# Kernel optimization log

Measured on AMD Instinct MI355X. Metric: run time of the kernel, lower is better.

Reference implementation:

```python
import jax, jax.numpy as jnp
import numpy as np

N = 100000      # nodes
E = 1600000     # edges
F_IN = 64       # CFG.feature_dim
H = 128         # CFG.hidden_dim
G = 128         # graphs in batch
LN_EPS = 1e-5


def setup_inputs() -> dict:
    key = jax.random.key(0)
    ks = jax.random.split(key, 12)
    x = jax.random.normal(ks[0], (N, F_IN), dtype=jnp.float32)
    edge_index = jax.random.randint(ks[1], (2, E), 0, N)
    batch = jnp.sort(jax.random.randint(ks[2], (N,), 0, G))
    # GCNConv weights (glorot-ish scale) and biases
    W1 = jax.random.normal(ks[3], (F_IN, H), dtype=jnp.float32) * (1.0 / np.sqrt(F_IN))
    b1 = jnp.zeros((H,), jnp.float32)
    W2 = jax.random.normal(ks[4], (H, H), dtype=jnp.float32) * (1.0 / np.sqrt(H))
    b2 = jnp.zeros((H,), jnp.float32)
    # LayerNorm affine params
    g1 = jnp.ones((H,), jnp.float32)
    beta1 = jnp.zeros((H,), jnp.float32)
    g2 = jnp.ones((H,), jnp.float32)
    beta2 = jnp.zeros((H,), jnp.float32)
    return {"x": x, "edge_index": edge_index, "batch": batch,
            "W1": W1, "b1": b1, "g1": g1, "beta1": beta1,
            "W2": W2, "b2": b2, "g2": g2, "beta2": beta2,
            "num_graphs": G}


def _gcn_conv(h, W, b, src, dst, n):
    """PyG GCNConv: add self-loops, symmetric D^-1/2 (A+I) D^-1/2 (h W) + b."""
    hw = h @ W                                   # [n, out]
    loop = jnp.arange(n, dtype=src.dtype)
    s = jnp.concatenate([src, loop])             # [E+n]
    d = jnp.concatenate([dst, loop])
    deg = jax.ops.segment_sum(jnp.ones_like(s, jnp.float32), d, num_segments=n)
    dinv = jax.lax.rsqrt(jnp.maximum(deg, 1e-12))
    norm = dinv[s] * dinv[d]                     # [E+n]
    msg = hw[s] * norm[:, None]                  # gather + scale
    out = jax.ops.segment_sum(msg, d, num_segments=n)
    return out + b


def _layer_norm(h, gamma, beta):
    mu = jnp.mean(h, axis=-1, keepdims=True)
    var = jnp.mean(jnp.square(h - mu), axis=-1, keepdims=True)
    return (h - mu) * jax.lax.rsqrt(var + LN_EPS) * gamma + beta


def reference(x, edge_index, batch, W1, b1, g1, beta1, W2, b2, g2, beta2, num_graphs):
    src, dst = edge_index[0], edge_index[1]
    n = x.shape[0]
    h = _gcn_conv(x, W1, b1, src, dst, n)
    h = _layer_norm(h, g1, beta1)
    h = jax.nn.relu(h)
    h = _gcn_conv(h, W2, b2, src, dst, n)
    h = _layer_norm(h, g2, beta2)
    # is_inverted defaults to False -> no sign flip
    sums = jax.ops.segment_sum(h, batch, num_segments=num_graphs)      # [G, H]
    counts = jax.ops.segment_sum(jnp.ones((n,), jnp.float32), batch, num_segments=num_graphs)
    return sums / jnp.maximum(counts, 1.0)[:, None]
```

## Files before the change

### kernel.cpp

```cpp
#include <hip/hip_runtime.h>
#include <hip/hip_bf16.h>

#define LN_EPS 1e-5f

typedef __attribute__((ext_vector_type(8))) short short8v;
typedef __attribute__((ext_vector_type(4))) float float4v;

__device__ __forceinline__ float bflo(unsigned u) { return __uint_as_float(u << 16); }
__device__ __forceinline__ float bfhi(unsigned u) { return __uint_as_float(u & 0xffff0000u); }
__device__ __forceinline__ unsigned pack2(float x, float y) {
    __hip_bfloat162 t = __float22bfloat162_rn(make_float2(x, y));
    return *reinterpret_cast<unsigned*>(&t);
}
__device__ __forceinline__ void add8(float* a, uint4 u) {
    a[0] += bflo(u.x); a[1] += bfhi(u.x);
    a[2] += bflo(u.y); a[3] += bfhi(u.y);
    a[4] += bflo(u.z); a[5] += bfhi(u.z);
    a[6] += bflo(u.w); a[7] += bfhi(u.w);
}

union U4S8 { uint4 u; short8v s; };


#define CHUNK 4096
#define NBMAX 512
#define BCAP 5120

__launch_bounds__(256)
__global__ void k_bucket(const int* __restrict__ src, const int* __restrict__ dst, int e,
                         int* __restrict__ gcnt, unsigned* __restrict__ stage) {
    __shared__ unsigned ebuf[CHUNK];
    __shared__ unsigned short ebkt[CHUNK];
    __shared__ int hist[NBMAX];
    __shared__ int base[NBMAX];
    int tid = threadIdx.x;
    int c0 = blockIdx.x * CHUNK;
    if (c0 >= e) return;
    int cnt = min(CHUNK, e - c0);

    for (int t = tid; t < NBMAX; t += 256) hist[t] = 0;
    __syncthreads();
    for (int t = tid; t < cnt; t += 256) {
        unsigned s = (unsigned)src[c0 + t];
        unsigned d = (unsigned)dst[c0 + t];
        ebuf[t] = s | ((d & 0xffu) << 24);
        ebkt[t] = (unsigned short)(d >> 8);
        atomicAdd(&hist[d >> 8], 1);
    }
    __syncthreads();
    for (int b = tid; b < NBMAX; b += 256) {
        int h = hist[b];
        if (h > 0) base[b] = b * BCAP + atomicAdd(&gcnt[b], h);
    }
    __syncthreads();
    for (int t = tid; t < cnt; t += 256) {
        int p = atomicAdd(&base[ebkt[t]], 1);
        stage[p] = ebuf[t];
    }
}

__launch_bounds__(256)
__global__ void k_csr(const unsigned* __restrict__ stage, const int* __restrict__ gcnt,
                      int* __restrict__ csr_src, int* __restrict__ row_start,
                      int* __restrict__ row_end, float* __restrict__ dinv,
                      const float* __restrict__ x, unsigned* __restrict__ xb, int n) {
    __shared__ int cntl[256];
    __shared__ int sc[256];
    __shared__ int excl[256];
    __shared__ float dfl[256];
    int b = blockIdx.x;
    int lo = b << 8;
    int nn = min(n - lo, 256);
    int tid = threadIdx.x;
    int s0 = b * BCAP;
    int cntB = gcnt[b];

    cntl[tid] = 0;
    __syncthreads();
    for (int t = tid; t < cntB; t += 256) {
        int dl = (int)(stage[s0 + t] >> 24);
        atomicAdd(&cntl[dl], 1);
    }
    __syncthreads();
    int deg = (tid < nn) ? cntl[tid] : 0;
    sc[tid] = deg; __syncthreads();
    for (int o = 1; o < 256; o <<= 1) {
        int t = (tid >= o) ? sc[tid - o] : 0;
        __syncthreads();
        sc[tid] += t;
        __syncthreads();
    }
    excl[tid] = sc[tid] - deg;
    float dv = rsqrtf((float)(deg + 1));
    dfl[tid] = dv;
    if (tid < nn) {
        row_start[lo + tid] = s0 + excl[tid];
        row_end[lo + tid]   = s0 + excl[tid] + deg;
        dinv[lo + tid] = dv;
    }
    cntl[tid] = 0;
    __syncthreads();
    for (int t = tid; t < cntB; t += 256) {
        unsigned ed = stage[s0 + t];
        int dl = (int)(ed >> 24);
        int r = atomicAdd(&cntl[dl], 1);
        csr_src[s0 + excl[dl] + r] = (int)(ed & 0x00ffffffu);
    }

    const float4* x4 = (const float4*)x;
    uint2* xb2 = (uint2*)xb;
    for (int idx = tid; idx < nn * 16; idx += 256) {
        int node = idx >> 4, c = idx & 15;
        size_t p = ((size_t)(lo + node) << 4) + c;
        float4 v = x4[p];
        float d = dfl[node];
        xb2[p] = make_uint2(pack2(v.x * d, v.y * d), pack2(v.z * d, v.w * d));
    }
}

__global__ void k_rc(const int* __restrict__ batch, int n, float* __restrict__ rc) {
    int g = threadIdx.x;
    int lo = 0, hi = n;
    while (lo < hi) { int m = (lo + hi) >> 1; if (batch[m] < g) lo = m + 1; else hi = m; }
    int st = lo;
    hi = n;
    while (lo < hi) { int m = (lo + hi) >> 1; if (batch[m] < g + 1) lo = m + 1; else hi = m; }
    rc[g] = 1.f / fmaxf((float)(lo - st), 1.f);
}


__global__ void k_agg64b(const uint4* __restrict__ x4, const float* __restrict__ dinv,
                         const int* __restrict__ row_start, const int* __restrict__ row_end,
                         const int* __restrict__ csr_src, uint4* __restrict__ out4, int n) {
    int lane = threadIdx.x & 63;
    int g = lane >> 3, c = lane & 7;
    int wid = (blockIdx.x * blockDim.x + threadIdx.x) >> 6;
    int nw = (gridDim.x * blockDim.x) >> 6;
    for (int i = wid; i < n; i += nw) {
        float a[8] = {0.f, 0.f, 0.f, 0.f, 0.f, 0.f, 0.f, 0.f};
        if (g == 0) {
            uint4 su = x4[(size_t)i * 8 + c];
            add8(a, su);
        }
        int j0 = row_start[i], j1 = row_end[i];
        int j = j0 + g;
        for (; j + 8 < j1; j += 16) {
            int s0 = csr_src[j], s1 = csr_src[j + 8];
            uint4 u0 = x4[(size_t)s0 * 8 + c];
            uint4 u1 = x4[(size_t)s1 * 8 + c];
            add8(a, u0);
            add8(a, u1);
        }
        if (j < j1) {
            int s0 = csr_src[j];
            uint4 u0 = x4[(size_t)s0 * 8 + c];
            add8(a, u0);
        }
        #pragma unroll
        for (int k = 0; k < 8; ++k) {
            a[k] += __shfl_xor(a[k], 8);
            a[k] += __shfl_xor(a[k], 16);
            a[k] += __shfl_xor(a[k], 32);
        }
        if (g == 0) {
            float di = dinv[i];
            uint4 o;
            o.x = pack2(a[0] * di, a[1] * di);
            o.y = pack2(a[2] * di, a[3] * di);
            o.z = pack2(a[4] * di, a[5] * di);
            o.w = pack2(a[6] * di, a[7] * di);
            out4[(size_t)i * 8 + c] = o;
        }
    }
}

__global__ void k_agg128b(const uint4* __restrict__ h4, const float* __restrict__ dinv,
                          const int* __restrict__ row_start, const int* __restrict__ row_end,
                          const int* __restrict__ csr_src, uint4* __restrict__ out4, int n) {
    int lane = threadIdx.x & 63;
    int q = lane >> 4, c = lane & 15;
    int wid = (blockIdx.x * blockDim.x + threadIdx.x) >> 6;
    int nw = (gridDim.x * blockDim.x) >> 6;
    for (int i = wid; i < n; i += nw) {
        float a[8] = {0.f, 0.f, 0.f, 0.f, 0.f, 0.f, 0.f, 0.f};
        if (q == 0) {
            uint4 su = h4[(size_t)i * 16 + c];
            add8(a, su);
        }
        int j0 = row_start[i], j1 = row_end[i];
        int j = j0 + q;
        for (; j + 12 < j1; j += 16) {
            int s0 = csr_src[j], s1 = csr_src[j + 4];
            int s2 = csr_src[j + 8], s3 = csr_src[j + 12];
            uint4 u0 = h4[(size_t)s0 * 16 + c];
            uint4 u1 = h4[(size_t)s1 * 16 + c];
            uint4 u2 = h4[(size_t)s2 * 16 + c];
            uint4 u3 = h4[(size_t)s3 * 16 + c];
            add8(a, u0);
            add8(a, u1);
            add8(a, u2);
            add8(a, u3);
        }
        for (; j < j1; j += 4) {
            int s0 = csr_src[j];
            uint4 u0 = h4[(size_t)s0 * 16 + c];
            add8(a, u0);
        }
        #pragma unroll
        for (int k = 0; k < 8; ++k) {
            a[k] += __shfl_xor(a[k], 16);
            a[k] += __shfl_xor(a[k], 32);
        }
        if (q == 0) {
            float di = dinv[i];
            uint4 o;
            o.x = pack2(a[0] * di, a[1] * di);
            o.y = pack2(a[2] * di, a[3] * di);
            o.z = pack2(a[4] * di, a[5] * di);
            o.w = pack2(a[6] * di, a[7] * di);
            out4[(size_t)i * 16 + c] = o;
        }
    }
}


__launch_bounds__(256)
__global__ void k_mm1(const unsigned* __restrict__ aggb, const float* __restrict__ W1,
                      const float* __restrict__ b1, const float* __restrict__ g1,
                      const float* __restrict__ be1, const float* __restrict__ dinv,
                      uint4* __restrict__ hb4, int ntiles) {
    __shared__ uint4 sB[2 * 8 * 64];
    for (int idx = threadIdx.x; idx < 1024; idx += blockDim.x) {
        int l = idx & 63;
        int f = idx >> 6;
        int ks = f >> 3, cb = f & 7;
        int kb = ks * 32 + (l >> 4) * 8;
        int col = cb * 16 + (l & 15);
        float p[8];
        #pragma unroll
        for (int j = 0; j < 8; ++j) p[j] = W1[(kb + j) * 128 + col];
        uint4 v;
        v.x = pack2(p[0], p[1]); v.y = pack2(p[2], p[3]);
        v.z = pack2(p[4], p[5]); v.w = pack2(p[6], p[7]);
        sB[idx] = v;
    }
    __syncthreads();

    int lane = threadIdx.x & 63;
    int wv = threadIdx.x >> 6;
    int wpb = blockDim.x >> 6;
    int lc = lane & 15, lg = lane >> 4;

    U4S8 B[2][8];
    #pragma unroll
    for (int ks = 0; ks < 2; ++ks)
        #pragma unroll
        for (int cb = 0; cb < 8; ++cb)
            B[ks][cb].u = sB[(ks * 8 + cb) * 64 + lane];

    float bs[8], gm[8], bt[8];
    #pragma unroll
    for (int cb = 0; cb < 8; ++cb) {
        bs[cb] = b1[cb * 16 + lc];
        gm[cb] = g1[cb * 16 + lc];
        bt[cb] = be1[cb * 16 + lc];
    }

    for (int t = blockIdx.x * wpb + wv; t < ntiles; t += gridDim.x * wpb) {
        size_t arow = (size_t)(t * 16 + lc) * 32;
        U4S8 a0, a1;
        a0.u = *(const uint4*)&aggb[arow + lg * 4];
        a1.u = *(const uint4*)&aggb[arow + 16 + lg * 4];
        float4v acc[8];
        #pragma unroll
        for (int cb = 0; cb < 8; ++cb) acc[cb] = (float4v){0.f, 0.f, 0.f, 0.f};
        #pragma unroll
        for (int cb = 0; cb < 8; ++cb) {
            acc[cb] = __builtin_amdgcn_mfma_f32_16x16x32_bf16(a0.s, B[0][cb].s, acc[cb], 0, 0, 0);
            acc[cb] = __builtin_amdgcn_mfma_f32_16x16x32_bf16(a1.s, B[1][cb].s, acc[cb], 0, 0, 0);
        }
        #pragma unroll
        for (int reg = 0; reg < 4; ++reg) {
            float s = 0.f, q = 0.f;
            #pragma unroll
            for (int cb = 0; cb < 8; ++cb) {
                float v = acc[cb][reg] + bs[cb];
                acc[cb][reg] = v;
                s += v; q = fmaf(v, v, q);
            }
            s += __shfl_xor(s, 1); q += __shfl_xor(q, 1);
            s += __shfl_xor(s, 2); q += __shfl_xor(q, 2);
            s += __shfl_xor(s, 4); q += __shfl_xor(q, 4);
            s += __shfl_xor(s, 8); q += __shfl_xor(q, 8);
            float mu = s * (1.f / 128.f);
            float var = fmaf(q, 1.f / 128.f, -mu * mu);
            float rstd = rsqrtf(var + LN_EPS);
            int rowi = t * 16 + lg * 4 + reg;
            float di = dinv[rowi];
            float o[8];
            #pragma unroll
            for (int cb = 0; cb < 8; ++cb)
                o[cb] = fmaxf(fmaf((acc[cb][reg] - mu) * rstd, gm[cb], bt[cb]), 0.f) * di;
            uint4 st;
            st.x = pack2(o[0], o[1]);
            st.y = pack2(o[2], o[3]);
            st.z = pack2(o[4], o[5]);
            st.w = pack2(o[6], o[7]);
            hb4[(size_t)rowi * 16 + lc] = st;
        }
    }
}

__launch_bounds__(256)
__global__ void k_mm2p(const unsigned* __restrict__ aggb, const float* __restrict__ W2,
                       const float* __restrict__ b2, const float* __restrict__ g2,
                       const float* __restrict__ be2, const int* __restrict__ batch,
                       const float* __restrict__ rc, float* __restrict__ psum, int ntiles) {
    __shared__ uint4 sB[4 * 8 * 64];
    for (int idx = threadIdx.x; idx < 2048; idx += blockDim.x) {
        int l = idx & 63;
        int f = idx >> 6;
        int ks = f >> 3, cb = f & 7;
        int lg = l >> 4;
        int col = cb * 16 + (l & 15);
        float p[8];
        #pragma unroll
        for (int j = 0; j < 8; ++j)
            p[j] = W2[(j * 16 + ks * 4 + lg) * 128 + col];
        uint4 v;
        v.x = pack2(p[0], p[1]); v.y = pack2(p[2], p[3]);
        v.z = pack2(p[4], p[5]); v.w = pack2(p[6], p[7]);
        sB[idx] = v;
    }
    __syncthreads();

    int lane = threadIdx.x & 63;
    int wv = threadIdx.x >> 6;
    int wpb = blockDim.x >> 6;
    int lc = lane & 15, lg = lane >> 4;
    float bs[8], gm[8], bt[8];
    #pragma unroll
    for (int cb = 0; cb < 8; ++cb) {
        bs[cb] = b2[cb * 16 + lc];
        gm[cb] = g2[cb * 16 + lc];
        bt[cb] = be2[cb * 16 + lc];
    }

    for (int t = blockIdx.x * wpb + wv; t < ntiles; t += gridDim.x * wpb) {
        int row0 = t * 16;
        size_t arow = (size_t)(row0 + lc) * 64;
        U4S8 a[4];
        #pragma unroll
        for (int ks = 0; ks < 4; ++ks)
            a[ks].u = *(const uint4*)&aggb[arow + ks * 16 + lg * 4];
        float4v acc[8];
        #pragma unroll
        for (int cb = 0; cb < 8; ++cb) acc[cb] = (float4v){0.f, 0.f, 0.f, 0.f};
        #pragma unroll
        for (int ks = 0; ks < 4; ++ks) {
            #pragma unroll
            for (int cb = 0; cb < 8; ++cb) {
                U4S8 fb;
                fb.u = sB[(ks * 8 + cb) * 64 + lane];
                acc[cb] = __builtin_amdgcn_mfma_f32_16x16x32_bf16(a[ks].s, fb.s, acc[cb], 0, 0, 0);
            }
        }
        #pragma unroll
        for (int reg = 0; reg < 4; ++reg) {
            float s = 0.f, q = 0.f;
            #pragma unroll
            for (int cb = 0; cb < 8; ++cb) {
                float v = acc[cb][reg] + bs[cb];
                acc[cb][reg] = v;
                s += v; q = fmaf(v, v, q);
            }
            s += __shfl_xor(s, 1); q += __shfl_xor(q, 1);
            s += __shfl_xor(s, 2); q += __shfl_xor(q, 2);
            s += __shfl_xor(s, 4); q += __shfl_xor(q, 4);
            s += __shfl_xor(s, 8); q += __shfl_xor(q, 8);
            float mu = s * (1.f / 128.f);
            float var = fmaf(q, 1.f / 128.f, -mu * mu);
            float rstd = rsqrtf(var + LN_EPS);
            #pragma unroll
            for (int cb = 0; cb < 8; ++cb)
                acc[cb][reg] = fmaf((acc[cb][reg] - mu) * rstd, gm[cb], bt[cb]);
        }
        int gmin = batch[row0];
        int gmax = batch[row0 + 15];
        int rg[4];
        #pragma unroll
        for (int reg = 0; reg < 4; ++reg) rg[reg] = batch[row0 + lg * 4 + reg];
        for (int g = gmin; g <= gmax; ++g) {
            float rcg = rc[g];
            #pragma unroll
            for (int cb = 0; cb < 8; ++cb) {
                float s = 0.f;
                #pragma unroll
                for (int reg = 0; reg < 4; ++reg)
                    s += (rg[reg] == g) ? acc[cb][reg] : 0.f;
                s += __shfl_xor(s, 16);
                s += __shfl_xor(s, 32);
                if (lg == 0) atomicAdd(&psum[g * 128 + cb * 16 + lc], s * rcg);
            }
        }
    }
}


extern "C" void kernel_launch(void* const* d_in, const int* in_sizes, int n_in,
                              void* d_out, int out_size, void* d_ws, size_t ws_size,
                              hipStream_t stream) {
    const float* x   = (const float*)d_in[0];
    const int*   ei  = (const int*)d_in[1];
    const int*   bat = (const int*)d_in[2];
    const float* W1  = (const float*)d_in[3];
    const float* b1  = (const float*)d_in[4];
    const float* g1  = (const float*)d_in[5];
    const float* be1 = (const float*)d_in[6];
    const float* W2  = (const float*)d_in[7];
    const float* b2  = (const float*)d_in[8];
    const float* g2  = (const float*)d_in[9];
    const float* be2 = (const float*)d_in[10];

    int n = in_sizes[0] / 64;
    int e = in_sizes[1] / 2;
    int G = out_size / 128;
    const int* src = ei;
    const int* dst = ei + e;

    int nbuckets = (n + 255) / 256;

    char* ws = (char*)d_ws;
    size_t off = 0;
    auto take = [&](size_t bytes) -> void* {
        void* p = ws + off;
        off = (off + bytes + 255) & ~(size_t)255;
        return p;
    };
    float*    dinv      = (float*)   take((size_t)n * 4);
    int*      row_start = (int*)     take((size_t)n * 4);
    int*      row_end   = (int*)     take((size_t)n * 4);
    int*      gcnt      = (int*)     take(NBMAX * 4);
    float*    rcbuf     = (float*)   take((size_t)G * 4);
    unsigned* stage     = (unsigned*)take((size_t)nbuckets * BCAP * 4);
    int*      csr_src   = (int*)     take((size_t)nbuckets * BCAP * 4);
    unsigned* xb        = (unsigned*)take((size_t)n * 64 * 2);
    unsigned* aggb      = (unsigned*)take((size_t)n * 64 * 2);
    unsigned* hb        = (unsigned*)take((size_t)n * 128 * 2);
    unsigned* agg2b     = (unsigned*)take((size_t)n * 128 * 2);

    hipMemsetAsync(gcnt, 0, NBMAX * 4, stream);
    hipMemsetAsync(d_out, 0, (size_t)out_size * 4, stream);

    int nbk = (e + CHUNK - 1) / CHUNK;
    k_bucket<<<nbk, 256, 0, stream>>>(src, dst, e, gcnt, stage);
    k_csr<<<nbuckets, 256, 0, stream>>>(stage, gcnt, csr_src, row_start, row_end,
                                        dinv, x, xb, n);
    k_rc<<<1, G, 0, stream>>>(bat, n, rcbuf);

    k_agg64b<<<2048, 256, 0, stream>>>((const uint4*)xb, dinv, row_start, row_end,
                                       csr_src, (uint4*)aggb, n);

    int ntiles = n / 16;
    k_mm1<<<626, 256, 0, stream>>>(aggb, W1, b1, g1, be1, dinv,
                                   (uint4*)hb, ntiles);

    k_agg128b<<<2048, 256, 0, stream>>>((const uint4*)hb, dinv, row_start, row_end,
                                        csr_src, (uint4*)agg2b, n);

    k_mm2p<<<626, 256, 0, stream>>>(agg2b, W2, b2, g2, be2, bat, rcbuf,
                                    (float*)d_out, ntiles);
}
```

Baseline: 215.5 us.

## Fuse neighbor aggregation into MFMA matmul kernels for both GCN layers

Merges each sparse aggregation kernel with the following MFMA matmul+LayerNorm kernel: each wave aggregates its 16 rows in turn and moves the packed bf16 results into MFMA A-operand registers via lane shuffles. This drops the aggb/agg2b intermediate buffers and their global write/read round trips, plus two kernel launches. In exchange each wave processes rows serially inside a tile, with extra shuffles and a different grid (one wave per tile). Load balance and latency hiding of the gather may change compared with the separate grid-stride aggregation kernels.

```diff
diff --git a/kernel.cpp b/kernel.cpp
--- a/kernel.cpp
+++ b/kernel.cpp
@@ -17,6 +17,14 @@
     a[2] += bflo(u.y); a[3] += bfhi(u.y);
     a[4] += bflo(u.z); a[5] += bfhi(u.z);
     a[6] += bflo(u.w); a[7] += bfhi(u.w);
+}
+__device__ __forceinline__ uint4 shfl4(uint4 v, int srcLane) {
+    uint4 r;
+    r.x = (unsigned)__shfl((int)v.x, srcLane);
+    r.y = (unsigned)__shfl((int)v.y, srcLane);
+    r.z = (unsigned)__shfl((int)v.z, srcLane);
+    r.w = (unsigned)__shfl((int)v.w, srcLane);
+    return r;
 }
 
 union U4S8 { uint4 u; short8v s; };
@@ -129,155 +137,93 @@
 }
 
 
-__global__ void k_agg64b(const uint4* __restrict__ x4, const float* __restrict__ dinv,
+__launch_bounds__(256)
+__global__ void k_f64mm1(const uint4* __restrict__ x4, const float* __restrict__ dinv,
                          const int* __restrict__ row_start, const int* __restrict__ row_end,
-                         const int* __restrict__ csr_src, uint4* __restrict__ out4, int n) {
+                         const int* __restrict__ csr_src,
+                         const float* __restrict__ W1, const float* __restrict__ b1,
+                         const float* __restrict__ g1, const float* __restrict__ be1,
+                         uint4* __restrict__ hb4, int ntiles) {
+    __shared__ uint4 sB[2 * 8 * 64];
+    for (int idx = threadIdx.x; idx < 1024; idx += 256) {
+        int l = idx & 63;
+        int f = idx >> 6;
+        int ks = f >> 3, cb = f & 7;
+        int kb = ks * 32 + (l >> 4) * 8;
+        int col = cb * 16 + (l & 15);
+        float p[8];
+        #pragma unroll
+        for (int j = 0; j < 8; ++j) p[j] = W1[(kb + j) * 128 + col];
+        uint4 v;
+        v.x = pack2(p[0], p[1]); v.y = pack2(p[2], p[3]);
+        v.z = pack2(p[4], p[5]); v.w = pack2(p[6], p[7]);
+        sB[idx] = v;
+    }
+    __syncthreads();
+
     int lane = threadIdx.x & 63;
-    int g = lane >> 3, c = lane & 7;
-    int wid = (blockIdx.x * blockDim.x + threadIdx.x) >> 6;
-    int nw = (gridDim.x * blockDim.x) >> 6;
-    for (int i = wid; i < n; i += nw) {
-        float a[8] = {0.f, 0.f, 0.f, 0.f, 0.f, 0.f, 0.f, 0.f};
-        if (g == 0) {
-            uint4 su = x4[(size_t)i * 8 + c];
-            add8(a, su);
-        }
-        int j0 = row_start[i], j1 = row_end[i];
-        int j = j0 + g;
-        for (; j + 8 < j1; j += 16) {
-            int s0 = csr_src[j], s1 = csr_src[j + 8];
-            uint4 u0 = x4[(size_t)s0 * 8 + c];
-            uint4 u1 = x4[(size_t)s1 * 8 + c];
-            add8(a, u0);
-            add8(a, u1);
-        }
-        if (j < j1) {
-            int s0 = csr_src[j];
-            uint4 u0 = x4[(size_t)s0 * 8 + c];
-            add8(a, u0);
-        }
-        #pragma unroll
-        for (int k = 0; k < 8; ++k) {
-            a[k] += __shfl_xor(a[k], 8);
-            a[k] += __shfl_xor(a[k], 16);
-            a[k] += __shfl_xor(a[k], 32);
-        }
-        if (g == 0) {
+    int lc = lane & 15, lg = lane >> 4;
+    int g8 = lane >> 3, c8 = lane & 7;
+    int gwave = blockIdx.x * 4 + (threadIdx.x >> 6);
+    int nwaves = gridDim.x * 4;
+
+    float bs[8], gm[8], bt[8];
+    #pragma unroll
+    for (int cb = 0; cb < 8; ++cb) {
+        bs[cb] = b1[cb * 16 + lc];
+        gm[cb] = g1[cb * 16 + lc];
+        bt[cb] = be1[cb * 16 + lc];
+    }
+
+    for (int t = gwave; t < ntiles; t += nwaves) {
+        U4S8 A0, A1;
+        for (int r = 0; r < 16; ++r) {
+            int i = t * 16 + r;
+            float a[8] = {0.f, 0.f, 0.f, 0.f, 0.f, 0.f, 0.f, 0.f};
+            if (g8 == 0) {
+                uint4 su = x4[(size_t)i * 8 + c8];
+                add8(a, su);
+            }
+            int j0 = row_start[i], j1 = row_end[i];
+            int j = j0 + g8;
+            for (; j + 8 < j1; j += 16) {
+                int s0 = csr_src[j], s1 = csr_src[j + 8];
+                uint4 u0 = x4[(size_t)s0 * 8 + c8];
+                uint4 u1 = x4[(size_t)s1 * 8 + c8];
+                add8(a, u0);
+                add8(a, u1);
+            }
+            if (j < j1) {
+                int s0 = csr_src[j];
+                uint4 u0 = x4[(size_t)s0 * 8 + c8];
+                add8(a, u0);
+            }
+            #pragma unroll
+            for (int k = 0; k < 8; ++k) {
+                a[k] += __shfl_xor(a[k], 8);
+                a[k] += __shfl_xor(a[k], 16);
+                a[k] += __shfl_xor(a[k], 32);
+            }
             float di = dinv[i];
             uint4 o;
             o.x = pack2(a[0] * di, a[1] * di);
             o.y = pack2(a[2] * di, a[3] * di);
             o.z = pack2(a[4] * di, a[5] * di);
             o.w = pack2(a[6] * di, a[7] * di);
-            out4[(size_t)i * 8 + c] = o;
-        }
-    }
-}
-
-__global__ void k_agg128b(const uint4* __restrict__ h4, const float* __restrict__ dinv,
-                          const int* __restrict__ row_start, const int* __restrict__ row_end,
-                          const int* __restrict__ csr_src, uint4* __restrict__ out4, int n) {
-    int lane = threadIdx.x & 63;
-    int q = lane >> 4, c = lane & 15;
-    int wid = (blockIdx.x * blockDim.x + threadIdx.x) >> 6;
-    int nw = (gridDim.x * blockDim.x) >> 6;
-    for (int i = wid; i < n; i += nw) {
-        float a[8] = {0.f, 0.f, 0.f, 0.f, 0.f, 0.f, 0.f, 0.f};
-        if (q == 0) {
-            uint4 su = h4[(size_t)i * 16 + c];
-            add8(a, su);
-        }
-        int j0 = row_start[i], j1 = row_end[i];
-        int j = j0 + q;
-        for (; j + 12 < j1; j += 16) {
-            int s0 = csr_src[j], s1 = csr_src[j + 4];
-            int s2 = csr_src[j + 8], s3 = csr_src[j + 12];
-            uint4 u0 = h4[(size_t)s0 * 16 + c];
-            uint4 u1 = h4[(size_t)s1 * 16 + c];
-            uint4 u2 = h4[(size_t)s2 * 16 + c];
-            uint4 u3 = h4[(size_t)s3 * 16 + c];
-            add8(a, u0);
-            add8(a, u1);
-            add8(a, u2);
-            add8(a, u3);
-        }
-        for (; j < j1; j += 4) {
-            int s0 = csr_src[j];
-            uint4 u0 = h4[(size_t)s0 * 16 + c];
-            add8(a, u0);
-        }
-        #pragma unroll
-        for (int k = 0; k < 8; ++k) {
-            a[k] += __shfl_xor(a[k], 16);
-            a[k] += __shfl_xor(a[k], 32);
-        }
-        if (q == 0) {
-            float di = dinv[i];
-            uint4 o;
-            o.x = pack2(a[0] * di, a[1] * di);
-            o.y = pack2(a[2] * di, a[3] * di);
-            o.z = pack2(a[4] * di, a[5] * di);
-            o.w = pack2(a[6] * di, a[7] * di);
-            out4[(size_t)i * 16 + c] = o;
-        }
-    }
-}
-
-
-__launch_bounds__(256)
-__global__ void k_mm1(const unsigned* __restrict__ aggb, const float* __restrict__ W1,
-                      const float* __restrict__ b1, const float* __restrict__ g1,
-                      const float* __restrict__ be1, const float* __restrict__ dinv,
-                      uint4* __restrict__ hb4, int ntiles) {
-    __shared__ uint4 sB[2 * 8 * 64];
-    for (int idx = threadIdx.x; idx < 1024; idx += blockDim.x) {
-        int l = idx & 63;
-        int f = idx >> 6;
-        int ks = f >> 3, cb = f & 7;
-        int kb = ks * 32 + (l >> 4) * 8;
-        int col = cb * 16 + (l & 15);
-        float p[8];
-        #pragma unroll
-        for (int j = 0; j < 8; ++j) p[j] = W1[(kb + j) * 128 + col];
-        uint4 v;
-        v.x = pack2(p[0], p[1]); v.y = pack2(p[2], p[3]);
-        v.z = pack2(p[4], p[5]); v.w = pack2(p[6], p[7]);
-        sB[idx] = v;
-    }
-    __syncthreads();
-
-    int lane = threadIdx.x & 63;
-    int wv = threadIdx.x >> 6;
-    int wpb = blockDim.x >> 6;
-    int lc = lane & 15, lg = lane >> 4;
-
-    U4S8 B[2][8];
-    #pragma unroll
-    for (int ks = 0; ks < 2; ++ks)
-        #pragma unroll
-        for (int cb = 0; cb < 8; ++cb)
-            B[ks][cb].u = sB[(ks * 8 + cb) * 64 + lane];
-
-    float bs[8], gm[8], bt[8];
-    #pragma unroll
-    for (int cb = 0; cb < 8; ++cb) {
-        bs[cb] = b1[cb * 16 + lc];
-        gm[cb] = g1[cb * 16 + lc];
-        bt[cb] = be1[cb * 16 + lc];
-    }
-
-    for (int t = blockIdx.x * wpb + wv; t < ntiles; t += gridDim.x * wpb) {
-        size_t arow = (size_t)(t * 16 + lc) * 32;
-        U4S8 a0, a1;
-        a0.u = *(const uint4*)&aggb[arow + lg * 4];
-        a1.u = *(const uint4*)&aggb[arow + 16 + lg * 4];
+            uint4 p0 = shfl4(o, lg);
+            uint4 p1 = shfl4(o, 4 + lg);
+            if (lc == r) { A0.u = p0; A1.u = p1; }
+        }
         float4v acc[8];
         #pragma unroll
         for (int cb = 0; cb < 8; ++cb) acc[cb] = (float4v){0.f, 0.f, 0.f, 0.f};
         #pragma unroll
         for (int cb = 0; cb < 8; ++cb) {
-            acc[cb] = __builtin_amdgcn_mfma_f32_16x16x32_bf16(a0.s, B[0][cb].s, acc[cb], 0, 0, 0);
-            acc[cb] = __builtin_amdgcn_mfma_f32_16x16x32_bf16(a1.s, B[1][cb].s, acc[cb], 0, 0, 0);
+            U4S8 f0, f1;
+            f0.u = sB[cb * 64 + lane];
+            f1.u = sB[(8 + cb) * 64 + lane];
+            acc[cb] = __builtin_amdgcn_mfma_f32_16x16x32_bf16(A0.s, f0.s, acc[cb], 0, 0, 0);
+            acc[cb] = __builtin_amdgcn_mfma_f32_16x16x32_bf16(A1.s, f1.s, acc[cb], 0, 0, 0);
         }
         #pragma unroll
         for (int reg = 0; reg < 4; ++reg) {
@@ -311,13 +257,17 @@
     }
 }
 
+
 __launch_bounds__(256)
-__global__ void k_mm2p(const unsigned* __restrict__ aggb, const float* __restrict__ W2,
-                       const float* __restrict__ b2, const float* __restrict__ g2,
-                       const float* __restrict__ be2, const int* __restrict__ batch,
-                       const float* __restrict__ rc, float* __restrict__ psum, int ntiles) {
+__global__ void k_f128mm2(const uint4* __restrict__ h4, const float* __restrict__ dinv,
+                          const int* __restrict__ row_start, const int* __restrict__ row_end,
+                          const int* __restrict__ csr_src,
+                          const float* __restrict__ W2, const float* __restrict__ b2,
+                          const float* __restrict__ g2, const float* __restrict__ be2,
+                          const int* __restrict__ batch, const float* __restrict__ rc,
+                          float* __restrict__ psum, int ntiles) {
     __shared__ uint4 sB[4 * 8 * 64];
-    for (int idx = threadIdx.x; idx < 2048; idx += blockDim.x) {
+    for (int idx = threadIdx.x; idx < 2048; idx += 256) {
         int l = idx & 63;
         int f = idx >> 6;
         int ks = f >> 3, cb = f & 7;
@@ -335,9 +285,10 @@
     __syncthreads();
 
     int lane = threadIdx.x & 63;
-    int wv = threadIdx.x >> 6;
-    int wpb = blockDim.x >> 6;
     int lc = lane & 15, lg = lane >> 4;
+    int gwave = blockIdx.x * 4 + (threadIdx.x >> 6);
+    int nwaves = gridDim.x * 4;
+
     float bs[8], gm[8], bt[8];
     #pragma unroll
     for (int cb = 0; cb < 8; ++cb) {
@@ -346,13 +297,51 @@
         bt[cb] = be2[cb * 16 + lc];
     }
 
-    for (int t = blockIdx.x * wpb + wv; t < ntiles; t += gridDim.x * wpb) {
-        int row0 = t * 16;
-        size_t arow = (size_t)(row0 + lc) * 64;
-        U4S8 a[4];
-        #pragma unroll
-        for (int ks = 0; ks < 4; ++ks)
-            a[ks].u = *(const uint4*)&aggb[arow + ks * 16 + lg * 4];
+    for (int t = gwave; t < ntiles; t += nwaves) {
+        U4S8 A[4];
+        for (int r = 0; r < 16; ++r) {
+            int i = t * 16 + r;
+            float a[8] = {0.f, 0.f, 0.f, 0.f, 0.f, 0.f, 0.f, 0.f};
+            if (lg == 0) {
+                uint4 su = h4[(size_t)i * 16 + lc];
+                add8(a, su);
+            }
+            int j0 = row_start[i], j1 = row_end[i];
+            int j = j0 + lg;
+            for (; j + 12 < j1; j += 16) {
+                int s0 = csr_src[j], s1 = csr_src[j + 4];
+                int s2 = csr_src[j + 8], s3 = csr_src[j + 12];
+                uint4 u0 = h4[(size_t)s0 * 16 + lc];
+                uint4 u1 = h4[(size_t)s1 * 16 + lc];
+                uint4 u2 = h4[(size_t)s2 * 16 + lc];
+                uint4 u3 = h4[(size_t)s3 * 16 + lc];
+                add8(a, u0);
+                add8(a, u1);
+                add8(a, u2);
+                add8(a, u3);
+            }
+            for (; j < j1; j += 4) {
+                int s0 = csr_src[j];
+                uint4 u0 = h4[(size_t)s0 * 16 + lc];
+                add8(a, u0);
+            }
+            #pragma unroll
+            for (int k = 0; k < 8; ++k) {
+                a[k] += __shfl_xor(a[k], 16);
+                a[k] += __shfl_xor(a[k], 32);
+            }
+            float di = dinv[i];
+            uint4 o;
+            o.x = pack2(a[0] * di, a[1] * di);
+            o.y = pack2(a[2] * di, a[3] * di);
+            o.z = pack2(a[4] * di, a[5] * di);
+            o.w = pack2(a[6] * di, a[7] * di);
+            #pragma unroll
+            for (int ks = 0; ks < 4; ++ks) {
+                uint4 pk = shfl4(o, ks * 4 + lg);
+                if (lc == r) A[ks].u = pk;
+            }
+        }
         float4v acc[8];
         #pragma unroll
         for (int cb = 0; cb < 8; ++cb) acc[cb] = (float4v){0.f, 0.f, 0.f, 0.f};
@@ -362,7 +351,7 @@
             for (int cb = 0; cb < 8; ++cb) {
                 U4S8 fb;
                 fb.u = sB[(ks * 8 + cb) * 64 + lane];
-                acc[cb] = __builtin_amdgcn_mfma_f32_16x16x32_bf16(a[ks].s, fb.s, acc[cb], 0, 0, 0);
+                acc[cb] = __builtin_amdgcn_mfma_f32_16x16x32_bf16(A[ks].s, fb.s, acc[cb], 0, 0, 0);
             }
         }
         #pragma unroll
@@ -385,6 +374,7 @@
             for (int cb = 0; cb < 8; ++cb)
                 acc[cb][reg] = fmaf((acc[cb][reg] - mu) * rstd, gm[cb], bt[cb]);
         }
+        int row0 = t * 16;
         int gmin = batch[row0];
         int gmax = batch[row0 + 15];
         int rg[4];
@@ -445,9 +435,7 @@
     unsigned* stage     = (unsigned*)take((size_t)nbuckets * BCAP * 4);
     int*      csr_src   = (int*)     take((size_t)nbuckets * BCAP * 4);
     unsigned* xb        = (unsigned*)take((size_t)n * 64 * 2);
-    unsigned* aggb      = (unsigned*)take((size_t)n * 64 * 2);
     unsigned* hb        = (unsigned*)take((size_t)n * 128 * 2);
-    unsigned* agg2b     = (unsigned*)take((size_t)n * 128 * 2);
 
     hipMemsetAsync(gcnt, 0, NBMAX * 4, stream);
     hipMemsetAsync(d_out, 0, (size_t)out_size * 4, stream);
@@ -458,16 +446,14 @@
                                         dinv, x, xb, n);
     k_rc<<<1, G, 0, stream>>>(bat, n, rcbuf);
 
-    k_agg64b<<<2048, 256, 0, stream>>>((const uint4*)xb, dinv, row_start, row_end,
-                                       csr_src, (uint4*)aggb, n);
-
     int ntiles = n / 16;
-    k_mm1<<<626, 256, 0, stream>>>(aggb, W1, b1, g1, be1, dinv,
-                                   (uint4*)hb, ntiles);
-
-    k_agg128b<<<2048, 256, 0, stream>>>((const uint4*)hb, dinv, row_start, row_end,
-                                        csr_src, (uint4*)agg2b, n);
-
-    k_mm2p<<<626, 256, 0, stream>>>(agg2b, W2, b2, g2, be2, bat, rcbuf,
-                                    (float*)d_out, ntiles);
-}
+    int fblocks = (ntiles + 3) / 4;
+
+    k_f64mm1<<<fblocks, 256, 0, stream>>>((const uint4*)xb, dinv, row_start, row_end,
+                                          csr_src, W1, b1, g1, be1,
+                                          (uint4*)hb, ntiles);
+
+    k_f128mm2<<<fblocks, 256, 0, stream>>>((const uint4*)hb, dinv, row_start, row_end,
+                                           csr_src, W2, b2, g2, be2, bat, rcbuf,
+                                           (float*)d_out, ntiles);
+}
```

After: 547.5 us. +154.0%, slower.
